# Performance work log

Hardware: AMD Instinct MI355X
Metric: run time of the kernel (lower is better)

The kernel has to match this reference:

```python
import jax, jax.numpy as jnp
import numpy as np

HEAD = 16

def setup_inputs() -> dict:
    key = jax.random.key(0)
    kq, kk, kv = jax.random.split(key, 3)
    B, S, D = 2, 2048, 1024
    q = jax.random.normal(kq, (B, S, D), dtype=jnp.float32)
    k = jax.random.normal(kk, (B, S, D), dtype=jnp.float32)
    v = jax.random.normal(kv, (B, S, D), dtype=jnp.float32)
    return {"q": q, "k": k, "v": v}

def reference(q, k, v):
    # NOTE: the source module overwrites the projected q1/k1/v1 with the raw
    # inputs (q1 = q, etc.), so w_q/w_k/w_v/w_o never affect the output.
    B, S, D = q.shape
    H = HEAD
    hd = D // H
    # [B, S, D] -> [B, H, S, hd]
    qh = q.reshape(B, S, H, hd).transpose(0, 2, 1, 3)
    kh = k.reshape(B, S, H, hd).transpose(0, 2, 1, 3)
    vh = v.reshape(B, S, H, hd).transpose(0, 2, 1, 3)
    scale = 1.0 / jnp.sqrt(jnp.float32(hd))
    scores = jnp.einsum('bhqd,bhkd->bhqk', qh, kh) * scale  # [B, H, S, S]
    attn = jax.nn.softmax(scores, axis=-1)
    x = jnp.einsum('bhqk,bhkd->bhqd', attn, vh)             # [B, H, S, hd]
    return x.transpose(0, 2, 1, 3).reshape(B, S, D)
```

## Files before the change

kernel.cpp:

```cpp
#include <hip/hip_runtime.h>
#include <hip/hip_bf16.h>

typedef __attribute__((ext_vector_type(8)))  __bf16 bf16x8;
typedef __attribute__((ext_vector_type(4)))  __bf16 bf16x4;
typedef __attribute__((ext_vector_type(4)))  float  f32x4;
typedef __attribute__((ext_vector_type(16))) float  f32x16;

#define S_LEN    2048
#define D_MODEL  1024
#define NH       16
#define HD       64
#define QB       128
#define NTILE    32
#define NOUTER   16
#define C_SCALE  0.18033688011112042f

static __device__ __forceinline__ f32x16 mfma32(bf16x8 a, bf16x8 b, f32x16 c) {
    return __builtin_amdgcn_mfma_f32_32x32x16_bf16(a, b, c, 0, 0, 0);
}

static __device__ __forceinline__ void gload16(const void* g, void* l) {
    __builtin_amdgcn_global_load_lds(
        (const __attribute__((address_space(1))) void*)g,
        (__attribute__((address_space(3)))       void*)l, 16, 0, 0);
}

__global__ __launch_bounds__(256, 4)
void prep_kernel(const float* __restrict__ Kp, const float* __restrict__ Vp,
                 char* __restrict__ Kb, char* __restrict__ Vb)
{
    const int bid  = blockIdx.x;
    const int bh   = bid >> 5;
    const int tile = bid & 31;
    const int b = bh >> 4, h = bh & 15;
    const int tid = threadIdx.x;
    const size_t gbase = (size_t)b * S_LEN * D_MODEL + (size_t)h * HD;
    char* kout = Kb + (size_t)bid * 8192;
    char* vout = Vb + (size_t)bid * 8192;

    {
        const int krow = tid >> 2, c2 = tid & 3;
        const float* kp = Kp + gbase + (size_t)(tile * 64 + krow) * D_MODEL + c2 * 16;
        f32x4 x0 = *(const f32x4*)(kp);
        f32x4 x1 = *(const f32x4*)(kp + 4);
        f32x4 x2 = *(const f32x4*)(kp + 8);
        f32x4 x3 = *(const f32x4*)(kp + 12);
        bf16x8 f0, f1;
        #pragma unroll
        for (int j = 0; j < 4; ++j) {
            f0[j] = (__bf16)x0[j]; f0[j + 4] = (__bf16)x1[j];
            f1[j] = (__bf16)x2[j]; f1[j + 4] = (__bf16)x3[j];
        }
        const int sw = (krow & 7) << 4;
        *(bf16x8*)(kout + krow * 128 + ((c2 * 32)      ^ sw)) = f0;
        *(bf16x8*)(kout + krow * 128 + ((c2 * 32 + 16) ^ sw)) = f1;
    }
    {
        const int vkg = tid >> 4, vdg = tid & 15;
        const float* vp = Vp + gbase + (size_t)(tile * 64 + vkg * 4) * D_MODEL + vdg * 4;
        f32x4 r0 = *(const f32x4*)(vp);
        f32x4 r1 = *(const f32x4*)(vp + D_MODEL);
        f32x4 r2 = *(const f32x4*)(vp + 2 * D_MODEL);
        f32x4 r3 = *(const f32x4*)(vp + 3 * D_MODEL);
        const int kvoff = 8 * ((vkg >> 1) & 1) + 16 * (vkg & 1) + 32 * (vkg >> 2);
        #pragma unroll
        for (int c = 0; c < 4; ++c) {
            const int d = vdg * 4 + c;
            bf16x4 pk;
            pk[0] = (__bf16)r0[c]; pk[1] = (__bf16)r1[c];
            pk[2] = (__bf16)r2[c]; pk[3] = (__bf16)r3[c];
            *(bf16x4*)(vout + d * 128 + (kvoff ^ ((d & 7) << 4))) = pk;
        }
    }
}

__global__ __launch_bounds__(256, 2)
void attn_kernel(const float* __restrict__ Qp, const char* __restrict__ Kb,
                 const char* __restrict__ Vb, float* __restrict__ Op)
{
    __shared__ __align__(16) char smem[65536];

    const int bid = blockIdx.x;
    const int bh = bid & 31, qtile = bid >> 5;
    const int b = bh >> 4, h = bh & 15;
    const int tid = threadIdx.x;
    const int w = tid >> 6, lane = tid & 63;
    const int ql = lane & 31, hi = lane >> 5;
    const int qp = w & 1, kh = w >> 1;

    const size_t gbase = (size_t)b * S_LEN * D_MODEL + (size_t)h * HD;

    bf16x8 qf[2][4];
    #pragma unroll
    for (int sub = 0; sub < 2; ++sub) {
        const int qrow = qtile * QB + qp * 64 + sub * 32 + ql;
        const float* qp_ = Qp + gbase + (size_t)qrow * D_MODEL + hi * 8;
        #pragma unroll
        for (int ks = 0; ks < 4; ++ks) {
            f32x4 a = *(const f32x4*)(qp_ + ks * 16);
            f32x4 c = *(const f32x4*)(qp_ + ks * 16 + 4);
            bf16x8 f;
            #pragma unroll
            for (int j = 0; j < 4; ++j) {
                f[j]     = (__bf16)(a[j] * C_SCALE);
                f[j + 4] = (__bf16)(c[j] * C_SCALE);
            }
            qf[sub][ks] = f;
        }
    }

    const char* kg0 = Kb + (size_t)(bh * NTILE) * 8192;
    const char* vg0 = Vb + (size_t)(bh * NTILE) * 8192;

    auto stage = [&](int db, int t) {
        const char* kg = kg0 + (size_t)t * 16384;
        const char* vg = vg0 + (size_t)t * 16384;
        char* kl = smem + db * 16384;
        char* vl = smem + 32768 + db * 16384;
        #pragma unroll
        for (int j = 0; j < 4; ++j) {
            const int o = j * 4096 + tid * 16;
            gload16(kg + o, kl + o);
            gload16(vg + o, vl + o);
        }
    };

    f32x16 oa0 = {0,0,0,0,0,0,0,0,0,0,0,0,0,0,0,0};
    f32x16 ob0 = {0,0,0,0,0,0,0,0,0,0,0,0,0,0,0,0};
    f32x16 oa1 = {0,0,0,0,0,0,0,0,0,0,0,0,0,0,0,0};
    f32x16 ob1 = {0,0,0,0,0,0,0,0,0,0,0,0,0,0,0,0};
    f32x4 l4a = {0.f, 0.f, 0.f, 0.f};
    f32x4 l4b = {0.f, 0.f, 0.f, 0.f};

    auto soft = [](const f32x16& sv, bf16x8* dst, f32x4& lacc) {
        float p[16];
        #pragma unroll
        for (int i = 0; i < 16; ++i) {
            p[i] = __builtin_amdgcn_exp2f(sv[i]);
            lacc[i & 3] += p[i];
        }
        #pragma unroll
        for (int z = 0; z < 2; ++z) {
            bf16x8 f;
            #pragma unroll
            for (int j = 0; j < 8; ++j) f[j] = (__bf16)p[z * 8 + j];
            dst[z] = f;
        }
    };

    stage(0, 0);
    int cur = 0;
    for (int t = 0; t < NOUTER; ++t) {
        __syncthreads();
        if (t + 1 < NOUTER) stage(cur ^ 1, t + 1);

        const char* kl = smem + cur * 16384 + kh * 8192;
        const char* vl = smem + 32768 + cur * 16384 + kh * 8192;

        f32x16 s00 = {0,0,0,0,0,0,0,0,0,0,0,0,0,0,0,0};
        f32x16 s01 = {0,0,0,0,0,0,0,0,0,0,0,0,0,0,0,0};
        f32x16 s10 = {0,0,0,0,0,0,0,0,0,0,0,0,0,0,0,0};
        f32x16 s11 = {0,0,0,0,0,0,0,0,0,0,0,0,0,0,0,0};
        __builtin_amdgcn_s_setprio(1);
        #pragma unroll
        for (int ks = 0; ks < 4; ++ks) {
            const int col = 32 * ks + 16 * hi;
            const int r0 = ql, r1 = 32 + ql;
            bf16x8 k0 = *(const bf16x8*)(kl + r0 * 128 + (col ^ ((r0 & 7) << 4)));
            bf16x8 k1 = *(const bf16x8*)(kl + r1 * 128 + (col ^ ((r1 & 7) << 4)));
            s00 = mfma32(k0, qf[0][ks], s00);
            s01 = mfma32(k1, qf[0][ks], s01);
            s10 = mfma32(k0, qf[1][ks], s10);
            s11 = mfma32(k1, qf[1][ks], s11);
        }
        __builtin_amdgcn_s_setprio(0);

        bf16x8 pa0[4], pa1[4];
        soft(s00, &pa0[0], l4a);
        soft(s01, &pa0[2], l4a);
        soft(s10, &pa1[0], l4b);
        soft(s11, &pa1[2], l4b);

        __builtin_amdgcn_s_setprio(1);
        #pragma unroll
        for (int ks = 0; ks < 4; ++ks) {
            const int col = 32 * ks + 16 * hi;
            const int d0 = ql, d1 = 32 + ql;
            bf16x8 v0 = *(const bf16x8*)(vl + d0 * 128 + (col ^ ((d0 & 7) << 4)));
            bf16x8 v1 = *(const bf16x8*)(vl + d1 * 128 + (col ^ ((d1 & 7) << 4)));
            oa0 = mfma32(pa0[ks], v0, oa0);
            ob0 = mfma32(pa0[ks], v1, ob0);
            oa1 = mfma32(pa1[ks], v0, oa1);
            ob1 = mfma32(pa1[ks], v1, ob1);
        }
        __builtin_amdgcn_s_setprio(0);
        cur ^= 1;
    }

    float lsA = (l4a[0] + l4a[1]) + (l4a[2] + l4a[3]);
    float lsB = (l4b[0] + l4b[1]) + (l4b[2] + l4b[3]);
    lsA += __shfl_xor(lsA, 32);
    lsB += __shfl_xor(lsB, 32);
    __syncthreads();
    float* lbuf = (float*)(smem + 32768);
    float* obuf = (float*)smem;
    const int qs0 = qp * 2, qs1 = qp * 2 + 1;
    if (lane < 32) {
        lbuf[kh * 128 + qs0 * 32 + ql] = lsA;
        lbuf[kh * 128 + qs1 * 32 + ql] = lsB;
    }
    __syncthreads();
    if (kh == 1) {
        #pragma unroll
        for (int i = 0; i < 16; ++i) {
            const int qloc = (i & 3) + 8 * (i >> 2) + 4 * hi;
            obuf[qs0 * 2048 + qloc * 64 + ql]      = oa0[i];
            obuf[qs0 * 2048 + qloc * 64 + 32 + ql] = ob0[i];
            obuf[qs1 * 2048 + qloc * 64 + ql]      = oa1[i];
            obuf[qs1 * 2048 + qloc * 64 + 32 + ql] = ob1[i];
        }
    }
    __syncthreads();
    if (kh == 0) {
        #pragma unroll
        for (int i = 0; i < 16; ++i) {
            const int qloc = (i & 3) + 8 * (i >> 2) + 4 * hi;
            const float ltA = lbuf[qs0 * 32 + qloc] + lbuf[128 + qs0 * 32 + qloc];
            const float ltB = lbuf[qs1 * 32 + qloc] + lbuf[128 + qs1 * 32 + qloc];
            const float invA = 1.0f / ltA;
            const float invB = 1.0f / ltB;
            float* opA = Op + gbase + (size_t)(qtile * QB + qs0 * 32 + qloc) * D_MODEL;
            float* opB = Op + gbase + (size_t)(qtile * QB + qs1 * 32 + qloc) * D_MODEL;
            opA[ql]      = (oa0[i] + obuf[qs0 * 2048 + qloc * 64 + ql])      * invA;
            opA[32 + ql] = (ob0[i] + obuf[qs0 * 2048 + qloc * 64 + 32 + ql]) * invA;
            opB[ql]      = (oa1[i] + obuf[qs1 * 2048 + qloc * 64 + ql])      * invB;
            opB[32 + ql] = (ob1[i] + obuf[qs1 * 2048 + qloc * 64 + 32 + ql]) * invB;
        }
    }
}

extern "C" void kernel_launch(void* const* d_in, const int* in_sizes, int n_in,
                              void* d_out, int out_size, void* d_ws, size_t ws_size,
                              hipStream_t stream) {
    const float* q = (const float*)d_in[0];
    const float* k = (const float*)d_in[1];
    const float* v = (const float*)d_in[2];
    float* out = (float*)d_out;
    char* Kb = (char*)d_ws;
    char* Vb = (char*)d_ws + 8 * 1024 * 1024;

    prep_kernel<<<dim3(32 * NTILE), dim3(256), 0, stream>>>(k, v, Kb, Vb);
    attn_kernel<<<dim3(32 * (S_LEN / QB)), dim3(256), 0, stream>>>(q, Kb, Vb, out);
}
```

Before: 58.05 us.

## Read K/V fragments directly from global memory, drop LDS staging, split keys across four waves

The prep kernel now writes K and V into an MFMA-fragment-friendly slab layout, staging through LDS and then writing coalesced. The attention kernel no longer double-buffers K/V tiles in shared memory. Each wave reads its fragments straight from global/L2 and owns a quarter of the keys for a 64-row query tile, and the four partial outputs are reduced serially through LDS. This removes the LDS staging and the per-tile barriers, and the smaller shared footprint allows more blocks per CU. In exchange there is no reuse of K/V across waves, each wave's loads are exposed latency with no software prefetch, and the final reduction is serialised.

```diff
diff --git a/kernel.cpp b/kernel.cpp
--- a/kernel.cpp
+++ b/kernel.cpp
@@ -10,25 +10,22 @@
 #define D_MODEL  1024
 #define NH       16
 #define HD       64
-#define QB       128
+#define QB       64
 #define NTILE    32
-#define NOUTER   16
+#define NTW      8
 #define C_SCALE  0.18033688011112042f
 
 static __device__ __forceinline__ f32x16 mfma32(bf16x8 a, bf16x8 b, f32x16 c) {
     return __builtin_amdgcn_mfma_f32_32x32x16_bf16(a, b, c, 0, 0, 0);
-}
-
-static __device__ __forceinline__ void gload16(const void* g, void* l) {
-    __builtin_amdgcn_global_load_lds(
-        (const __attribute__((address_space(1))) void*)g,
-        (__attribute__((address_space(3)))       void*)l, 16, 0, 0);
 }
 
 __global__ __launch_bounds__(256, 4)
 void prep_kernel(const float* __restrict__ Kp, const float* __restrict__ Vp,
                  char* __restrict__ Kb, char* __restrict__ Vb)
 {
+    __shared__ __align__(16) char klds[8192];
+    __shared__ __align__(16) char vlds[8192];
+
     const int bid  = blockIdx.x;
     const int bh   = bid >> 5;
     const int tile = bid & 31;
@@ -51,9 +48,8 @@
             f0[j] = (__bf16)x0[j]; f0[j + 4] = (__bf16)x1[j];
             f1[j] = (__bf16)x2[j]; f1[j + 4] = (__bf16)x3[j];
         }
-        const int sw = (krow & 7) << 4;
-        *(bf16x8*)(kout + krow * 128 + ((c2 * 32)      ^ sw)) = f0;
-        *(bf16x8*)(kout + krow * 128 + ((c2 * 32 + 16) ^ sw)) = f1;
+        *(bf16x8*)(klds + (2 * c2 + 0) * 1024 + krow * 16) = f0;
+        *(bf16x8*)(klds + (2 * c2 + 1) * 1024 + krow * 16) = f1;
     }
     {
         const int vkg = tid >> 4, vdg = tid & 15;
@@ -69,8 +65,17 @@
             bf16x4 pk;
             pk[0] = (__bf16)r0[c]; pk[1] = (__bf16)r1[c];
             pk[2] = (__bf16)r2[c]; pk[3] = (__bf16)r3[c];
-            *(bf16x4*)(vout + d * 128 + (kvoff ^ ((d & 7) << 4))) = pk;
-        }
+            *(bf16x4*)(vlds + (kvoff >> 4) * 1024 + d * 16 + (kvoff & 15)) = pk;
+        }
+    }
+    __syncthreads();
+    {
+        f32x4* ks = (f32x4*)(klds + tid * 32);
+        f32x4* vs = (f32x4*)(vlds + tid * 32);
+        f32x4* kd = (f32x4*)(kout + tid * 32);
+        f32x4* vd = (f32x4*)(vout + tid * 32);
+        kd[0] = ks[0]; kd[1] = ks[1];
+        vd[0] = vs[0]; vd[1] = vs[1];
     }
 }
 
@@ -78,7 +83,8 @@
 void attn_kernel(const float* __restrict__ Qp, const char* __restrict__ Kb,
                  const char* __restrict__ Vb, float* __restrict__ Op)
 {
-    __shared__ __align__(16) char smem[65536];
+    __shared__ float lbuf[4 * 64];
+    __shared__ __align__(16) float obuf[64 * 64];
 
     const int bid = blockIdx.x;
     const int bh = bid & 31, qtile = bid >> 5;
@@ -86,14 +92,14 @@
     const int tid = threadIdx.x;
     const int w = tid >> 6, lane = tid & 63;
     const int ql = lane & 31, hi = lane >> 5;
-    const int qp = w & 1, kh = w >> 1;
+    const int kq = w;
 
     const size_t gbase = (size_t)b * S_LEN * D_MODEL + (size_t)h * HD;
 
     bf16x8 qf[2][4];
     #pragma unroll
     for (int sub = 0; sub < 2; ++sub) {
-        const int qrow = qtile * QB + qp * 64 + sub * 32 + ql;
+        const int qrow = qtile * QB + sub * 32 + ql;
         const float* qp_ = Qp + gbase + (size_t)qrow * D_MODEL + hi * 8;
         #pragma unroll
         for (int ks = 0; ks < 4; ++ks) {
@@ -109,21 +115,8 @@
         }
     }
 
-    const char* kg0 = Kb + (size_t)(bh * NTILE) * 8192;
-    const char* vg0 = Vb + (size_t)(bh * NTILE) * 8192;
-
-    auto stage = [&](int db, int t) {
-        const char* kg = kg0 + (size_t)t * 16384;
-        const char* vg = vg0 + (size_t)t * 16384;
-        char* kl = smem + db * 16384;
-        char* vl = smem + 32768 + db * 16384;
-        #pragma unroll
-        for (int j = 0; j < 4; ++j) {
-            const int o = j * 4096 + tid * 16;
-            gload16(kg + o, kl + o);
-            gload16(vg + o, vl + o);
-        }
-    };
+    const char* kg = Kb + (size_t)(bh * NTILE + kq * NTW) * 8192;
+    const char* vg = Vb + (size_t)(bh * NTILE + kq * NTW) * 8192;
 
     f32x16 oa0 = {0,0,0,0,0,0,0,0,0,0,0,0,0,0,0,0};
     f32x16 ob0 = {0,0,0,0,0,0,0,0,0,0,0,0,0,0,0,0};
@@ -148,14 +141,9 @@
         }
     };
 
-    stage(0, 0);
-    int cur = 0;
-    for (int t = 0; t < NOUTER; ++t) {
-        __syncthreads();
-        if (t + 1 < NOUTER) stage(cur ^ 1, t + 1);
-
-        const char* kl = smem + cur * 16384 + kh * 8192;
-        const char* vl = smem + 32768 + cur * 16384 + kh * 8192;
+    for (int i = 0; i < NTW; ++i) {
+        const char* kt = kg + i * 8192;
+        const char* vt = vg + i * 8192;
 
         f32x16 s00 = {0,0,0,0,0,0,0,0,0,0,0,0,0,0,0,0};
         f32x16 s01 = {0,0,0,0,0,0,0,0,0,0,0,0,0,0,0,0};
@@ -164,10 +152,9 @@
         __builtin_amdgcn_s_setprio(1);
         #pragma unroll
         for (int ks = 0; ks < 4; ++ks) {
-            const int col = 32 * ks + 16 * hi;
-            const int r0 = ql, r1 = 32 + ql;
-            bf16x8 k0 = *(const bf16x8*)(kl + r0 * 128 + (col ^ ((r0 & 7) << 4)));
-            bf16x8 k1 = *(const bf16x8*)(kl + r1 * 128 + (col ^ ((r1 & 7) << 4)));
+            const int sl = (2 * ks + hi) * 1024;
+            bf16x8 k0 = *(const bf16x8*)(kt + sl + ql * 16);
+            bf16x8 k1 = *(const bf16x8*)(kt + sl + (32 + ql) * 16);
             s00 = mfma32(k0, qf[0][ks], s00);
             s01 = mfma32(k1, qf[0][ks], s01);
             s10 = mfma32(k0, qf[1][ks], s10);
@@ -184,57 +171,97 @@
         __builtin_amdgcn_s_setprio(1);
         #pragma unroll
         for (int ks = 0; ks < 4; ++ks) {
-            const int col = 32 * ks + 16 * hi;
-            const int d0 = ql, d1 = 32 + ql;
-            bf16x8 v0 = *(const bf16x8*)(vl + d0 * 128 + (col ^ ((d0 & 7) << 4)));
-            bf16x8 v1 = *(const bf16x8*)(vl + d1 * 128 + (col ^ ((d1 & 7) << 4)));
+            const int sl = (2 * ks + hi) * 1024;
+            bf16x8 v0 = *(const bf16x8*)(vt + sl + ql * 16);
+            bf16x8 v1 = *(const bf16x8*)(vt + sl + (32 + ql) * 16);
             oa0 = mfma32(pa0[ks], v0, oa0);
             ob0 = mfma32(pa0[ks], v1, ob0);
             oa1 = mfma32(pa1[ks], v0, oa1);
             ob1 = mfma32(pa1[ks], v1, ob1);
         }
         __builtin_amdgcn_s_setprio(0);
-        cur ^= 1;
     }
 
     float lsA = (l4a[0] + l4a[1]) + (l4a[2] + l4a[3]);
     float lsB = (l4b[0] + l4b[1]) + (l4b[2] + l4b[3]);
     lsA += __shfl_xor(lsA, 32);
     lsB += __shfl_xor(lsB, 32);
-    __syncthreads();
-    float* lbuf = (float*)(smem + 32768);
-    float* obuf = (float*)smem;
-    const int qs0 = qp * 2, qs1 = qp * 2 + 1;
     if (lane < 32) {
-        lbuf[kh * 128 + qs0 * 32 + ql] = lsA;
-        lbuf[kh * 128 + qs1 * 32 + ql] = lsB;
-    }
-    __syncthreads();
-    if (kh == 1) {
-        #pragma unroll
-        for (int i = 0; i < 16; ++i) {
-            const int qloc = (i & 3) + 8 * (i >> 2) + 4 * hi;
-            obuf[qs0 * 2048 + qloc * 64 + ql]      = oa0[i];
-            obuf[qs0 * 2048 + qloc * 64 + 32 + ql] = ob0[i];
-            obuf[qs1 * 2048 + qloc * 64 + ql]      = oa1[i];
-            obuf[qs1 * 2048 + qloc * 64 + 32 + ql] = ob1[i];
-        }
-    }
-    __syncthreads();
-    if (kh == 0) {
-        #pragma unroll
-        for (int i = 0; i < 16; ++i) {
-            const int qloc = (i & 3) + 8 * (i >> 2) + 4 * hi;
-            const float ltA = lbuf[qs0 * 32 + qloc] + lbuf[128 + qs0 * 32 + qloc];
-            const float ltB = lbuf[qs1 * 32 + qloc] + lbuf[128 + qs1 * 32 + qloc];
+        lbuf[kq * 64 + ql]      = lsA;
+        lbuf[kq * 64 + 32 + ql] = lsB;
+    }
+    __syncthreads();
+    if (kq == 1) {
+        #pragma unroll
+        for (int i = 0; i < 16; ++i) {
+            const int qloc = (i & 3) + 8 * (i >> 2) + 4 * hi;
+            obuf[qloc * 64 + ql]             = oa0[i];
+            obuf[qloc * 64 + 32 + ql]        = ob0[i];
+            obuf[(32 + qloc) * 64 + ql]      = oa1[i];
+            obuf[(32 + qloc) * 64 + 32 + ql] = ob1[i];
+        }
+    }
+    __syncthreads();
+    if (kq == 0) {
+        #pragma unroll
+        for (int i = 0; i < 16; ++i) {
+            const int qloc = (i & 3) + 8 * (i >> 2) + 4 * hi;
+            oa0[i] += obuf[qloc * 64 + ql];
+            ob0[i] += obuf[qloc * 64 + 32 + ql];
+            oa1[i] += obuf[(32 + qloc) * 64 + ql];
+            ob1[i] += obuf[(32 + qloc) * 64 + 32 + ql];
+        }
+    }
+    __syncthreads();
+    if (kq == 2) {
+        #pragma unroll
+        for (int i = 0; i < 16; ++i) {
+            const int qloc = (i & 3) + 8 * (i >> 2) + 4 * hi;
+            obuf[qloc * 64 + ql]             = oa0[i];
+            obuf[qloc * 64 + 32 + ql]        = ob0[i];
+            obuf[(32 + qloc) * 64 + ql]      = oa1[i];
+            obuf[(32 + qloc) * 64 + 32 + ql] = ob1[i];
+        }
+    }
+    __syncthreads();
+    if (kq == 0) {
+        #pragma unroll
+        for (int i = 0; i < 16; ++i) {
+            const int qloc = (i & 3) + 8 * (i >> 2) + 4 * hi;
+            oa0[i] += obuf[qloc * 64 + ql];
+            ob0[i] += obuf[qloc * 64 + 32 + ql];
+            oa1[i] += obuf[(32 + qloc) * 64 + ql];
+            ob1[i] += obuf[(32 + qloc) * 64 + 32 + ql];
+        }
+    }
+    __syncthreads();
+    if (kq == 3) {
+        #pragma unroll
+        for (int i = 0; i < 16; ++i) {
+            const int qloc = (i & 3) + 8 * (i >> 2) + 4 * hi;
+            obuf[qloc * 64 + ql]             = oa0[i];
+            obuf[qloc * 64 + 32 + ql]        = ob0[i];
+            obuf[(32 + qloc) * 64 + ql]      = oa1[i];
+            obuf[(32 + qloc) * 64 + 32 + ql] = ob1[i];
+        }
+    }
+    __syncthreads();
+    if (kq == 0) {
+        #pragma unroll
+        for (int i = 0; i < 16; ++i) {
+            const int qloc = (i & 3) + 8 * (i >> 2) + 4 * hi;
+            const float ltA = lbuf[qloc] + lbuf[64 + qloc] +
+                              lbuf[128 + qloc] + lbuf[192 + qloc];
+            const float ltB = lbuf[32 + qloc] + lbuf[96 + qloc] +
+                              lbuf[160 + qloc] + lbuf[224 + qloc];
             const float invA = 1.0f / ltA;
             const float invB = 1.0f / ltB;
-            float* opA = Op + gbase + (size_t)(qtile * QB + qs0 * 32 + qloc) * D_MODEL;
-            float* opB = Op + gbase + (size_t)(qtile * QB + qs1 * 32 + qloc) * D_MODEL;
-            opA[ql]      = (oa0[i] + obuf[qs0 * 2048 + qloc * 64 + ql])      * invA;
-            opA[32 + ql] = (ob0[i] + obuf[qs0 * 2048 + qloc * 64 + 32 + ql]) * invA;
-            opB[ql]      = (oa1[i] + obuf[qs1 * 2048 + qloc * 64 + ql])      * invB;
-            opB[32 + ql] = (ob1[i] + obuf[qs1 * 2048 + qloc * 64 + 32 + ql]) * invB;
+            float* opA = Op + gbase + (size_t)(qtile * QB + qloc) * D_MODEL;
+            float* opB = Op + gbase + (size_t)(qtile * QB + 32 + qloc) * D_MODEL;
+            opA[ql]      = (oa0[i] + obuf[qloc * 64 + ql])             * invA;
+            opA[32 + ql] = (ob0[i] + obuf[qloc * 64 + 32 + ql])        * invA;
+            opB[ql]      = (oa1[i] + obuf[(32 + qloc) * 64 + ql])      * invB;
+            opB[32 + ql] = (ob1[i] + obuf[(32 + qloc) * 64 + 32 + ql]) * invB;
         }
     }
 }
```

After: 65.32 us. 12.5% more time.
